# Optimization experiments

Hardware: AMD Instinct MI355X
Metric: run time of the kernel (lower is better)

## Reference

```python
import jax, jax.numpy as jnp
import numpy as np
from jax import lax

LEAKY_ALPHA = 0.2  # tf.nn.leaky_relu default


def setup_inputs() -> dict:
    key = jax.random.key(0)
    k1, k2, k3 = jax.random.split(key, 3)
    B, C, D, H, W = 8, 2, 96, 64, 64
    F, d, h, w = 8, 3, 60, 64
    inputs = jax.random.normal(k1, (B, C, D, H, W), dtype=jnp.float32)
    # weight/bias correspond to tf variables [F,1,c,d,h,w] with the singleton squeezed
    weight = jax.random.normal(k2, (F, C, d, h, w), dtype=jnp.float32) * 0.05
    bias = jax.random.normal(k3, (F, C, d, h, w), dtype=jnp.float32) * 0.05
    return {"inputs": inputs, "weight": weight, "bias": bias}


def reference(inputs, weight, bias):
    B, C, D, H, W = inputs.shape
    F, _, d, h, w = weight.shape
    margin = H - h
    Dout = D - d + 1  # depth positions where tf.slice succeeds

    # sliding depth windows: xwin[b,c,i,k,:,:] = inputs[b,c,i+k,:,:] -> [B,C,Dout,d,H,W]
    xwin = jnp.stack([inputs[:, :, k:k + Dout] for k in range(d)], axis=3)
    # margin accumulation over H (sum of margin+1 shifted h-slices): [B,C,Dout,d,h,W]
    s = xwin[..., 0:h, :]
    for j in range(1, margin + 1):
        s = s + xwin[..., j:j + h, :]
    s = jnp.moveaxis(s, 2, 1)  # [B,Dout,C,d,h,w]

    # y = (sum_j x_slice_j * w + b) * 0.25 -> a[b,f,i,c,k,p,q]
    a = (s[:, None] * weight[None, :, None] + bias[None, :, None]) * 0.25
    # a: [B,F,Dout,C,d,h,w]

    # fixed ones-kernel conv3d, filters=1, SAME, strides (d,1,1), then leaky_relu
    a_r = a.reshape(B * F * Dout, C, d, h, w)
    kernel = jnp.ones((1, C, 3, 3, 3), dtype=a_r.dtype)
    conv = lax.conv_general_dilated(
        a_r, kernel, window_strides=(d, 1, 1), padding='SAME',
        dimension_numbers=('NCDHW', 'OIDHW', 'NCDHW'))  # [N,1,1,h,w]
    out = jax.nn.leaky_relu(conv, negative_slope=LEAKY_ALPHA)
    return out.reshape(B, F, Dout, h, w)
```

## Files before the change

### kernel.cpp

```cpp
#include <hip/hip_runtime.h>

#define B_ 8
#define C_ 2
#define D_ 96
#define H_ 64
#define W_ 64
#define F_ 8
#define KD 3
#define h_ 60
#define Dout_ 94
#define PLANE (h_ * W_)
#define NCH (PLANE / 4)
#define TD 8
#define NTILE ((Dout_ + TD - 1) / TD)
#define S2_FLOATS ((size_t)B_ * C_ * D_ * PLANE)

__global__ __launch_bounds__(256) void k_s2(const float* __restrict__ in,
                                            float* __restrict__ s2) {
    const int bx = blockIdx.x;
    const float4* ip4 = (const float4*)(in + (size_t)bx * (H_ * W_));
    float4* op4 = (float4*)(s2 + (size_t)bx * PLANE);
    __shared__ float4 lds[H_ * 16];
    const int tid = threadIdx.x;
#pragma unroll
    for (int k = 0; k < 4; ++k) lds[tid + 256 * k] = ip4[tid + 256 * k];
    __syncthreads();
#pragma unroll
    for (int k = 0; k < 4; ++k) {
        const int e = tid + 256 * k;
        if (e < NCH) {
            const int row = e >> 4, col = e & 15;
            float4 s = lds[row * 16 + col];
#pragma unroll
            for (int j = 1; j < 5; ++j) {
                const float4 v = lds[(row + j) * 16 + col];
                s.x += v.x; s.y += v.y; s.z += v.z; s.w += v.w;
            }
            op4[e] = s;
        }
    }
}

__device__ __forceinline__ float4 hsum3(float4 V, int col4) {
    const int lane = threadIdx.x & 63;
    float lw = __shfl(V.w, (lane + 63) & 63, 64);
    float rx = __shfl(V.x, (lane + 1) & 63, 64);
    if (col4 == 0) lw = 0.f;
    if (col4 == 15) rx = 0.f;
    float4 o;
    o.x = lw + V.x + V.y;
    o.y = V.x + V.y + V.z;
    o.z = V.y + V.z + V.w;
    o.w = V.z + V.w + rx;
    return o;
}

__global__ __launch_bounds__(256) void k_boxbs(const float* __restrict__ bs,
                                               float* __restrict__ bb) {
    const int f = blockIdx.x;
    const int tid = threadIdx.x;
    __shared__ float4 R[62 * 16];
    if (tid < 32) {
        const int r = (tid >> 4) ? 61 : 0;
        R[r * 16 + (tid & 15)] = make_float4(0, 0, 0, 0);
    }
    const float4* bp = (const float4*)(bs + (size_t)f * (C_ * KD * PLANE));
#pragma unroll
    for (int k = 0; k < 4; ++k) {
        const int e = tid + 256 * k;
        if (e < NCH) {
            float4 s = make_float4(0, 0, 0, 0);
#pragma unroll
            for (int s6 = 0; s6 < 6; ++s6) {
                const float4 v = bp[s6 * NCH + e];
                s.x += v.x; s.y += v.y; s.z += v.z; s.w += v.w;
            }
            const int row = e >> 4, col = e & 15;
            R[(row + 1) * 16 + col] = s;
        }
    }
    __syncthreads();
    float4* ob = (float4*)(bb + (size_t)f * PLANE);
#pragma unroll
    for (int k = 0; k < 4; ++k) {
        const int e = tid + 256 * k;
        if (e < NCH) {
            const int row = e >> 4, c4 = e & 15;
            const float4 a = R[row * 16 + c4];
            const float4 m = R[(row + 1) * 16 + c4];
            const float4 d = R[(row + 2) * 16 + c4];
            float4 V;
            V.x = a.x + m.x + d.x; V.y = a.y + m.y + d.y;
            V.z = a.z + m.z + d.z; V.w = a.w + m.w + d.w;
            ob[e] = hsum3(V, c4);
        }
    }
}

__global__ __launch_bounds__(256) void k_main(const float* __restrict__ s2,
                                              const float* __restrict__ wt,
                                              const float* __restrict__ bb,
                                              float* __restrict__ out) {
    const int bx = blockIdx.x;
    const int tile = bx % NTILE;
    const int f = (bx / NTILE) % F_;
    const int b = bx / (NTILE * F_);
    const int d0 = tile * TD;
    const int tid = threadIdx.x;

    float4 wreg[6][4];
    const float4* wp = (const float4*)(wt + (size_t)f * (C_ * KD * PLANE));
#pragma unroll
    for (int s6 = 0; s6 < 6; ++s6)
#pragma unroll
        for (int k = 0; k < 4; ++k) {
            const int e = tid + 256 * k;
            wreg[s6][k] = (e < NCH) ? wp[s6 * NCH + e] : make_float4(0, 0, 0, 0);
        }

    __shared__ float4 R[62 * 16];
    if (tid < 32) {
        const int r = (tid >> 4) ? 61 : 0;
        R[r * 16 + (tid & 15)] = make_float4(0, 0, 0, 0);
    }

    const float4* s2b = (const float4*)s2 + (size_t)(b * C_) * D_ * NCH;
    const float4* bbp = (const float4*)(bb + (size_t)f * PLANE);
    float* ob = out + (size_t)((b * F_ + f) * Dout_) * PLANE;

    for (int t = 0; t < TD; ++t) {
        const int dout = d0 + t;
        if (dout >= Dout_) break;

        float4 acc[4];
#pragma unroll
        for (int k = 0; k < 4; ++k) acc[k] = make_float4(0, 0, 0, 0);

#pragma unroll
        for (int c = 0; c < C_; ++c)
#pragma unroll
            for (int z = 0; z < KD; ++z) {
                const float4* sp = s2b + (size_t)(c * D_ + dout + z) * NCH;
#pragma unroll
                for (int k = 0; k < 4; ++k) {
                    const int e = tid + 256 * k;
                    if (e < NCH) {
                        const float4 v = sp[e];
                        const float4 w = wreg[c * KD + z][k];
                        acc[k].x += v.x * w.x; acc[k].y += v.y * w.y;
                        acc[k].z += v.z * w.z; acc[k].w += v.w * w.w;
                    }
                }
            }

        if (t > 0) __syncthreads();
#pragma unroll
        for (int k = 0; k < 4; ++k) {
            const int e = tid + 256 * k;
            if (e < NCH) R[((e >> 4) + 1) * 16 + (e & 15)] = acc[k];
        }
        __syncthreads();

        float4* od4 = (float4*)(ob + (size_t)dout * PLANE);
#pragma unroll
        for (int k = 0; k < 4; ++k) {
            const int e = tid + 256 * k;
            if (e < NCH) {
                const int row = e >> 4, c4 = e & 15;
                const float4 a = R[row * 16 + c4];
                const float4 m = R[(row + 1) * 16 + c4];
                const float4 d = R[(row + 2) * 16 + c4];
                float4 V;
                V.x = a.x + m.x + d.x; V.y = a.y + m.y + d.y;
                V.z = a.z + m.z + d.z; V.w = a.w + m.w + d.w;
                float4 o = hsum3(V, c4);
                const float4 bbv = bbp[e];
                o.x = 0.25f * (o.x + bbv.x); o.y = 0.25f * (o.y + bbv.y);
                o.z = 0.25f * (o.z + bbv.z); o.w = 0.25f * (o.w + bbv.w);
                o.x = (o.x > 0.f) ? o.x : 0.2f * o.x;
                o.y = (o.y > 0.f) ? o.y : 0.2f * o.y;
                o.z = (o.z > 0.f) ? o.z : 0.2f * o.z;
                o.w = (o.w > 0.f) ? o.w : 0.2f * o.w;
                od4[e] = o;
            }
        }
    }
}

extern "C" void kernel_launch(void* const* d_in, const int* in_sizes, int n_in,
                              void* d_out, int out_size, void* d_ws, size_t ws_size,
                              hipStream_t stream) {
    const float* in = (const float*)d_in[0];
    const float* wt = (const float*)d_in[1];
    const float* bs = (const float*)d_in[2];
    float* out = (float*)d_out;

    float* s2 = (float*)d_ws;
    float* bb = s2 + S2_FLOATS;

    k_boxbs<<<dim3(F_), dim3(256), 0, stream>>>(bs, bb);
    k_s2<<<dim3(B_ * C_ * D_), dim3(256), 0, stream>>>(in, s2);
    k_main<<<dim3(B_ * F_ * NTILE), dim3(256), 0, stream>>>(s2, wt, bb, out);
}
```

Measured before the change: 168.4 us.

## Merge prep kernels, halve depth tile, double-buffer LDS and unroll main loop

Merges the s2 box-sum kernel and the bias box-filter kernel into one launch that dispatches on block index, which removes one kernel launch. In the main kernel, the depth tile drops from 8 to 4, giving twice as many blocks for more parallelism but more per-block weight register loads. The LDS staging buffer is double-buffered, so one barrier per step replaces two. The depth loop is fully unrolled with clamped reads instead of an early break. The cost is redundant weight reloads per block and extra clamped compute on the tail tile.

Result: no change. 165.2 us (-1.9%).

```diff
diff --git a/kernel.cpp b/kernel.cpp
--- a/kernel.cpp
+++ b/kernel.cpp
@@ -11,35 +11,10 @@
 #define Dout_ 94
 #define PLANE (h_ * W_)
 #define NCH (PLANE / 4)
-#define TD 8
+#define TD 4
 #define NTILE ((Dout_ + TD - 1) / TD)
-#define S2_FLOATS ((size_t)B_ * C_ * D_ * PLANE)
-
-__global__ __launch_bounds__(256) void k_s2(const float* __restrict__ in,
-                                            float* __restrict__ s2) {
-    const int bx = blockIdx.x;
-    const float4* ip4 = (const float4*)(in + (size_t)bx * (H_ * W_));
-    float4* op4 = (float4*)(s2 + (size_t)bx * PLANE);
-    __shared__ float4 lds[H_ * 16];
-    const int tid = threadIdx.x;
-#pragma unroll
-    for (int k = 0; k < 4; ++k) lds[tid + 256 * k] = ip4[tid + 256 * k];
-    __syncthreads();
-#pragma unroll
-    for (int k = 0; k < 4; ++k) {
-        const int e = tid + 256 * k;
-        if (e < NCH) {
-            const int row = e >> 4, col = e & 15;
-            float4 s = lds[row * 16 + col];
-#pragma unroll
-            for (int j = 1; j < 5; ++j) {
-                const float4 v = lds[(row + j) * 16 + col];
-                s.x += v.x; s.y += v.y; s.z += v.z; s.w += v.w;
-            }
-            op4[e] = s;
-        }
-    }
-}
+#define NS2 (B_ * C_ * D_)
+#define S2_FLOATS ((size_t)NS2 * PLANE)
 
 __device__ __forceinline__ float4 hsum3(float4 V, int col4) {
     const int lane = threadIdx.x & 63;
@@ -55,44 +30,70 @@
     return o;
 }
 
-__global__ __launch_bounds__(256) void k_boxbs(const float* __restrict__ bs,
-                                               float* __restrict__ bb) {
-    const int f = blockIdx.x;
+__global__ __launch_bounds__(256) void k_prep(const float* __restrict__ in,
+                                              const float* __restrict__ bs,
+                                              float* __restrict__ s2,
+                                              float* __restrict__ bb) {
+    const int bx = blockIdx.x;
     const int tid = threadIdx.x;
-    __shared__ float4 R[62 * 16];
-    if (tid < 32) {
-        const int r = (tid >> 4) ? 61 : 0;
-        R[r * 16 + (tid & 15)] = make_float4(0, 0, 0, 0);
-    }
-    const float4* bp = (const float4*)(bs + (size_t)f * (C_ * KD * PLANE));
-#pragma unroll
-    for (int k = 0; k < 4; ++k) {
-        const int e = tid + 256 * k;
-        if (e < NCH) {
-            float4 s = make_float4(0, 0, 0, 0);
-#pragma unroll
-            for (int s6 = 0; s6 < 6; ++s6) {
-                const float4 v = bp[s6 * NCH + e];
-                s.x += v.x; s.y += v.y; s.z += v.z; s.w += v.w;
-            }
-            const int row = e >> 4, col = e & 15;
-            R[(row + 1) * 16 + col] = s;
-        }
-    }
-    __syncthreads();
-    float4* ob = (float4*)(bb + (size_t)f * PLANE);
-#pragma unroll
-    for (int k = 0; k < 4; ++k) {
-        const int e = tid + 256 * k;
-        if (e < NCH) {
-            const int row = e >> 4, c4 = e & 15;
-            const float4 a = R[row * 16 + c4];
-            const float4 m = R[(row + 1) * 16 + c4];
-            const float4 d = R[(row + 2) * 16 + c4];
-            float4 V;
-            V.x = a.x + m.x + d.x; V.y = a.y + m.y + d.y;
-            V.z = a.z + m.z + d.z; V.w = a.w + m.w + d.w;
-            ob[e] = hsum3(V, c4);
+    __shared__ float4 lds[H_ * 16];
+
+    if (bx < NS2) {
+        const float4* ip4 = (const float4*)(in + (size_t)bx * (H_ * W_));
+        float4* op4 = (float4*)(s2 + (size_t)bx * PLANE);
+#pragma unroll
+        for (int k = 0; k < 4; ++k) lds[tid + 256 * k] = ip4[tid + 256 * k];
+        __syncthreads();
+#pragma unroll
+        for (int k = 0; k < 4; ++k) {
+            const int e = tid + 256 * k;
+            if (e < NCH) {
+                const int row = e >> 4, col = e & 15;
+                float4 s = lds[row * 16 + col];
+#pragma unroll
+                for (int j = 1; j < 5; ++j) {
+                    const float4 v = lds[(row + j) * 16 + col];
+                    s.x += v.x; s.y += v.y; s.z += v.z; s.w += v.w;
+                }
+                op4[e] = s;
+            }
+        }
+    } else {
+        const int f = bx - NS2;
+        float4* R = lds;
+        if (tid < 32) {
+            const int r = (tid >> 4) ? 61 : 0;
+            R[r * 16 + (tid & 15)] = make_float4(0, 0, 0, 0);
+        }
+        const float4* bp = (const float4*)(bs + (size_t)f * (C_ * KD * PLANE));
+#pragma unroll
+        for (int k = 0; k < 4; ++k) {
+            const int e = tid + 256 * k;
+            if (e < NCH) {
+                float4 s = make_float4(0, 0, 0, 0);
+#pragma unroll
+                for (int s6 = 0; s6 < 6; ++s6) {
+                    const float4 v = bp[s6 * NCH + e];
+                    s.x += v.x; s.y += v.y; s.z += v.z; s.w += v.w;
+                }
+                R[((e >> 4) + 1) * 16 + (e & 15)] = s;
+            }
+        }
+        __syncthreads();
+        float4* ob = (float4*)(bb + (size_t)f * PLANE);
+#pragma unroll
+        for (int k = 0; k < 4; ++k) {
+            const int e = tid + 256 * k;
+            if (e < NCH) {
+                const int row = e >> 4, c4 = e & 15;
+                const float4 a = R[row * 16 + c4];
+                const float4 m = R[(row + 1) * 16 + c4];
+                const float4 d = R[(row + 2) * 16 + c4];
+                float4 V;
+                V.x = a.x + m.x + d.x; V.y = a.y + m.y + d.y;
+                V.z = a.z + m.z + d.z; V.w = a.w + m.w + d.w;
+                ob[e] = hsum3(V, c4);
+            }
         }
     }
 }
@@ -118,19 +119,20 @@
             wreg[s6][k] = (e < NCH) ? wp[s6 * NCH + e] : make_float4(0, 0, 0, 0);
         }
 
-    __shared__ float4 R[62 * 16];
+    __shared__ float4 R[2][62 * 16];
     if (tid < 32) {
         const int r = (tid >> 4) ? 61 : 0;
-        R[r * 16 + (tid & 15)] = make_float4(0, 0, 0, 0);
+        R[0][r * 16 + (tid & 15)] = make_float4(0, 0, 0, 0);
+        R[1][r * 16 + (tid & 15)] = make_float4(0, 0, 0, 0);
     }
 
     const float4* s2b = (const float4*)s2 + (size_t)(b * C_) * D_ * NCH;
     const float4* bbp = (const float4*)(bb + (size_t)f * PLANE);
     float* ob = out + (size_t)((b * F_ + f) * Dout_) * PLANE;
 
+#pragma unroll
     for (int t = 0; t < TD; ++t) {
         const int dout = d0 + t;
-        if (dout >= Dout_) break;
 
         float4 acc[4];
 #pragma unroll
@@ -140,7 +142,8 @@
         for (int c = 0; c < C_; ++c)
 #pragma unroll
             for (int z = 0; z < KD; ++z) {
-                const float4* sp = s2b + (size_t)(c * D_ + dout + z) * NCH;
+                int p = dout + z; if (p > D_ - 1) p = D_ - 1;
+                const float4* sp = s2b + (size_t)(c * D_ + p) * NCH;
 #pragma unroll
                 for (int k = 0; k < 4; ++k) {
                     const int e = tid + 256 * k;
@@ -153,35 +156,37 @@
                 }
             }
 
-        if (t > 0) __syncthreads();
-#pragma unroll
-        for (int k = 0; k < 4; ++k) {
-            const int e = tid + 256 * k;
-            if (e < NCH) R[((e >> 4) + 1) * 16 + (e & 15)] = acc[k];
+        float4* Rb = R[t & 1];
+#pragma unroll
+        for (int k = 0; k < 4; ++k) {
+            const int e = tid + 256 * k;
+            if (e < NCH) Rb[((e >> 4) + 1) * 16 + (e & 15)] = acc[k];
         }
         __syncthreads();
 
-        float4* od4 = (float4*)(ob + (size_t)dout * PLANE);
-#pragma unroll
-        for (int k = 0; k < 4; ++k) {
-            const int e = tid + 256 * k;
-            if (e < NCH) {
-                const int row = e >> 4, c4 = e & 15;
-                const float4 a = R[row * 16 + c4];
-                const float4 m = R[(row + 1) * 16 + c4];
-                const float4 d = R[(row + 2) * 16 + c4];
-                float4 V;
-                V.x = a.x + m.x + d.x; V.y = a.y + m.y + d.y;
-                V.z = a.z + m.z + d.z; V.w = a.w + m.w + d.w;
-                float4 o = hsum3(V, c4);
-                const float4 bbv = bbp[e];
-                o.x = 0.25f * (o.x + bbv.x); o.y = 0.25f * (o.y + bbv.y);
-                o.z = 0.25f * (o.z + bbv.z); o.w = 0.25f * (o.w + bbv.w);
-                o.x = (o.x > 0.f) ? o.x : 0.2f * o.x;
-                o.y = (o.y > 0.f) ? o.y : 0.2f * o.y;
-                o.z = (o.z > 0.f) ? o.z : 0.2f * o.z;
-                o.w = (o.w > 0.f) ? o.w : 0.2f * o.w;
-                od4[e] = o;
+        if (dout < Dout_) {
+            float4* od4 = (float4*)(ob + (size_t)dout * PLANE);
+#pragma unroll
+            for (int k = 0; k < 4; ++k) {
+                const int e = tid + 256 * k;
+                if (e < NCH) {
+                    const int row = e >> 4, c4 = e & 15;
+                    const float4 a = Rb[row * 16 + c4];
+                    const float4 m = Rb[(row + 1) * 16 + c4];
+                    const float4 d = Rb[(row + 2) * 16 + c4];
+                    float4 V;
+                    V.x = a.x + m.x + d.x; V.y = a.y + m.y + d.y;
+                    V.z = a.z + m.z + d.z; V.w = a.w + m.w + d.w;
+                    float4 o = hsum3(V, c4);
+                    const float4 bbv = bbp[e];
+                    o.x = 0.25f * (o.x + bbv.x); o.y = 0.25f * (o.y + bbv.y);
+                    o.z = 0.25f * (o.z + bbv.z); o.w = 0.25f * (o.w + bbv.w);
+                    o.x = (o.x > 0.f) ? o.x : 0.2f * o.x;
+                    o.y = (o.y > 0.f) ? o.y : 0.2f * o.y;
+                    o.z = (o.z > 0.f) ? o.z : 0.2f * o.z;
+                    o.w = (o.w > 0.f) ? o.w : 0.2f * o.w;
+                    od4[e] = o;
+                }
             }
         }
     }
@@ -198,7 +203,6 @@
     float* s2 = (float*)d_ws;
     float* bb = s2 + S2_FLOATS;
 
-    k_boxbs<<<dim3(F_), dim3(256), 0, stream>>>(bs, bb);
-    k_s2<<<dim3(B_ * C_ * D_), dim3(256), 0, stream>>>(in, s2);
+    k_prep<<<dim3(NS2 + F_), dim3(256), 0, stream>>>(in, bs, s2, bb);
     k_main<<<dim3(B_ * F_ * NTILE), dim3(256), 0, stream>>>(s2, wt, bb, out);
 }
```

## Fuse margin-sum into main kernel and parallelize over batch and depth position

Applied to the files above, without the earlier changes.

The separate kernel that wrote the H-margin sums to a workspace is removed. The main kernel now loads each input plane into LDS, forms the margin sums in registers, and uses one 320-thread block per (batch, output depth). Each block loops over all filters and reads weights from global memory, ping-ponging two LDS buffers between the plane loads and the 3x3 box stage. This drops the workspace write and re-read and one launch. In exchange the full weight tensor is streamed through cache by every block, and the shuffle in the bias-box kernel now runs unconditionally so all lanes take part.

New measurement: 253.3 us. 50.4% more time.

```diff
diff --git a/kernel.cpp b/kernel.cpp
--- a/kernel.cpp
+++ b/kernel.cpp
@@ -11,42 +11,26 @@
 #define Dout_ 94
 #define PLANE (h_ * W_)
 #define NCH (PLANE / 4)
-#define TD 8
-#define NTILE ((Dout_ + TD - 1) / TD)
-#define S2_FLOATS ((size_t)B_ * C_ * D_ * PLANE)
+#define INCH (H_ * W_ / 4)
+#define NT 320
 
-__global__ __launch_bounds__(256) void k_s2(const float* __restrict__ in,
-                                            float* __restrict__ s2) {
-    const int bx = blockIdx.x;
-    const float4* ip4 = (const float4*)(in + (size_t)bx * (H_ * W_));
-    float4* op4 = (float4*)(s2 + (size_t)bx * PLANE);
-    __shared__ float4 lds[H_ * 16];
-    const int tid = threadIdx.x;
-#pragma unroll
-    for (int k = 0; k < 4; ++k) lds[tid + 256 * k] = ip4[tid + 256 * k];
-    __syncthreads();
-#pragma unroll
-    for (int k = 0; k < 4; ++k) {
-        const int e = tid + 256 * k;
-        if (e < NCH) {
-            const int row = e >> 4, col = e & 15;
-            float4 s = lds[row * 16 + col];
-#pragma unroll
-            for (int j = 1; j < 5; ++j) {
-                const float4 v = lds[(row + j) * 16 + col];
-                s.x += v.x; s.y += v.y; s.z += v.z; s.w += v.w;
-            }
-            op4[e] = s;
-        }
-    }
+__device__ __forceinline__ float4 f4fma(float4 a, float4 b, float4 c) {
+    c.x += a.x * b.x; c.y += a.y * b.y; c.z += a.z * b.z; c.w += a.w * b.w;
+    return c;
+}
+__device__ __forceinline__ float4 f4add3(float4 a, float4 b, float4 c) {
+    float4 o;
+    o.x = a.x + b.x + c.x; o.y = a.y + b.y + c.y;
+    o.z = a.z + b.z + c.z; o.w = a.w + b.w + c.w;
+    return o;
 }
 
-__device__ __forceinline__ float4 hsum3(float4 V, int col4) {
+__device__ __forceinline__ float4 hsum3(float4 V, int c4) {
     const int lane = threadIdx.x & 63;
     float lw = __shfl(V.w, (lane + 63) & 63, 64);
     float rx = __shfl(V.x, (lane + 1) & 63, 64);
-    if (col4 == 0) lw = 0.f;
-    if (col4 == 15) rx = 0.f;
+    if (c4 == 0) lw = 0.f;
+    if (c4 == 15) rx = 0.f;
     float4 o;
     o.x = lw + V.x + V.y;
     o.y = V.x + V.y + V.z;
@@ -55,8 +39,8 @@
     return o;
 }
 
-__global__ __launch_bounds__(256) void k_boxbs(const float* __restrict__ bs,
-                                               float* __restrict__ bb) {
+__global__ __launch_bounds__(256) void k_bb(const float* __restrict__ bs,
+                                            float* __restrict__ bb) {
     const int f = blockIdx.x;
     const int tid = threadIdx.x;
     __shared__ float4 R[62 * 16];
@@ -75,8 +59,7 @@
                 const float4 v = bp[s6 * NCH + e];
                 s.x += v.x; s.y += v.y; s.z += v.z; s.w += v.w;
             }
-            const int row = e >> 4, col = e & 15;
-            R[(row + 1) * 16 + col] = s;
+            R[((e >> 4) + 1) * 16 + (e & 15)] = s;
         }
     }
     __syncthreads();
@@ -84,105 +67,117 @@
 #pragma unroll
     for (int k = 0; k < 4; ++k) {
         const int e = tid + 256 * k;
+        float4 V = make_float4(0, 0, 0, 0);
+        int c4 = e & 15;
         if (e < NCH) {
-            const int row = e >> 4, c4 = e & 15;
-            const float4 a = R[row * 16 + c4];
-            const float4 m = R[(row + 1) * 16 + c4];
-            const float4 d = R[(row + 2) * 16 + c4];
-            float4 V;
-            V.x = a.x + m.x + d.x; V.y = a.y + m.y + d.y;
-            V.z = a.z + m.z + d.z; V.w = a.w + m.w + d.w;
-            ob[e] = hsum3(V, c4);
+            const int row = e >> 4;
+            V = f4add3(R[row * 16 + c4], R[(row + 1) * 16 + c4],
+                       R[(row + 2) * 16 + c4]);
         }
+        float4 o = hsum3(V, c4);
+        if (e < NCH) ob[e] = o;
     }
 }
 
-__global__ __launch_bounds__(256) void k_main(const float* __restrict__ s2,
-                                              const float* __restrict__ wt,
-                                              const float* __restrict__ bb,
-                                              float* __restrict__ out) {
+__global__ __launch_bounds__(NT) void k_main(const float* __restrict__ in,
+                                             const float* __restrict__ wt,
+                                             const float* __restrict__ bb,
+                                             float* __restrict__ out) {
     const int bx = blockIdx.x;
-    const int tile = bx % NTILE;
-    const int f = (bx / NTILE) % F_;
-    const int b = bx / (NTILE * F_);
-    const int d0 = tile * TD;
+    const int dout = bx % Dout_;
+    const int b = bx / Dout_;
     const int tid = threadIdx.x;
 
-    float4 wreg[6][4];
-    const float4* wp = (const float4*)(wt + (size_t)f * (C_ * KD * PLANE));
+    __shared__ float4 L[2][INCH];
+
+    int e[3], c4[3], row[3];
 #pragma unroll
-    for (int s6 = 0; s6 < 6; ++s6)
+    for (int k = 0; k < 3; ++k) {
+        e[k] = tid + NT * k;
+        row[k] = e[k] >> 4;
+        c4[k] = e[k] & 15;
+    }
+
+    float4 s2r[6][3];
+    const float4* in4 = (const float4*)in;
 #pragma unroll
-        for (int k = 0; k < 4; ++k) {
-            const int e = tid + 256 * k;
-            wreg[s6][k] = (e < NCH) ? wp[s6 * NCH + e] : make_float4(0, 0, 0, 0);
+    for (int c = 0; c < C_; ++c)
+#pragma unroll
+        for (int z = 0; z < KD; ++z) {
+            const int p = c * KD + z;
+            const size_t pb = ((size_t)(b * C_ + c) * D_ + (dout + z)) * INCH;
+            float4* Ls = L[p & 1];
+#pragma unroll
+            for (int k2 = 0; k2 < 4; ++k2) {
+                const int idx = tid + NT * k2;
+                if (idx < INCH) Ls[idx] = in4[pb + idx];
+            }
+            __syncthreads();
+#pragma unroll
+            for (int k = 0; k < 3; ++k) {
+                float4 s = Ls[row[k] * 16 + c4[k]];
+#pragma unroll
+                for (int j = 1; j < 5; ++j) {
+                    const float4 v = Ls[(row[k] + j) * 16 + c4[k]];
+                    s.x += v.x; s.y += v.y; s.z += v.z; s.w += v.w;
+                }
+                s2r[p][k] = s;
+            }
         }
 
-    __shared__ float4 R[62 * 16];
-    if (tid < 32) {
-        const int r = (tid >> 4) ? 61 : 0;
-        R[r * 16 + (tid & 15)] = make_float4(0, 0, 0, 0);
-    }
+    const float4* wt4 = (const float4*)wt;
+    const float4* bb4 = (const float4*)bb;
+    float4* out4 = (float4*)out;
+    const float4 z4 = make_float4(0, 0, 0, 0);
 
-    const float4* s2b = (const float4*)s2 + (size_t)(b * C_) * D_ * NCH;
-    const float4* bbp = (const float4*)(bb + (size_t)f * PLANE);
-    float* ob = out + (size_t)((b * F_ + f) * Dout_) * PLANE;
-
-    for (int t = 0; t < TD; ++t) {
-        const int dout = d0 + t;
-        if (dout >= Dout_) break;
-
-        float4 acc[4];
+    for (int f = 0; f < F_; ++f) {
+        float4 acc[3];
 #pragma unroll
-        for (int k = 0; k < 4; ++k) acc[k] = make_float4(0, 0, 0, 0);
+        for (int k = 0; k < 3; ++k) acc[k] = z4;
 
 #pragma unroll
         for (int c = 0; c < C_; ++c)
 #pragma unroll
             for (int z = 0; z < KD; ++z) {
-                const float4* sp = s2b + (size_t)(c * D_ + dout + z) * NCH;
+                const size_t wb = (size_t)((f * C_ + c) * KD + z) * NCH;
 #pragma unroll
-                for (int k = 0; k < 4; ++k) {
-                    const int e = tid + 256 * k;
-                    if (e < NCH) {
-                        const float4 v = sp[e];
-                        const float4 w = wreg[c * KD + z][k];
-                        acc[k].x += v.x * w.x; acc[k].y += v.y * w.y;
-                        acc[k].z += v.z * w.z; acc[k].w += v.w * w.w;
-                    }
+                for (int k = 0; k < 3; ++k) {
+                    const float4 w = wt4[wb + e[k]];
+                    acc[k] = f4fma(w, s2r[c * KD + z][k], acc[k]);
                 }
             }
 
-        if (t > 0) __syncthreads();
+        float4 bbv[3];
 #pragma unroll
-        for (int k = 0; k < 4; ++k) {
-            const int e = tid + 256 * k;
-            if (e < NCH) R[((e >> 4) + 1) * 16 + (e & 15)] = acc[k];
+        for (int k = 0; k < 3; ++k)
+            bbv[k] = bb4[(size_t)f * NCH + e[k]];
+
+        float4* Lb = L[f & 1];
+        if (f < 2 && tid < 32) {
+            const int r = (tid >> 4) ? 61 : 0;
+            Lb[r * 16 + (tid & 15)] = z4;
         }
+#pragma unroll
+        for (int k = 0; k < 3; ++k)
+            Lb[(row[k] + 1) * 16 + c4[k]] = acc[k];
         __syncthreads();
 
-        float4* od4 = (float4*)(ob + (size_t)dout * PLANE);
+        const size_t ob = ((size_t)(b * F_ + f) * Dout_ + dout) * NCH;
 #pragma unroll
-        for (int k = 0; k < 4; ++k) {
-            const int e = tid + 256 * k;
-            if (e < NCH) {
-                const int row = e >> 4, c4 = e & 15;
-                const float4 a = R[row * 16 + c4];
-                const float4 m = R[(row + 1) * 16 + c4];
-                const float4 d = R[(row + 2) * 16 + c4];
-                float4 V;
-                V.x = a.x + m.x + d.x; V.y = a.y + m.y + d.y;
-                V.z = a.z + m.z + d.z; V.w = a.w + m.w + d.w;
-                float4 o = hsum3(V, c4);
-                const float4 bbv = bbp[e];
-                o.x = 0.25f * (o.x + bbv.x); o.y = 0.25f * (o.y + bbv.y);
-                o.z = 0.25f * (o.z + bbv.z); o.w = 0.25f * (o.w + bbv.w);
-                o.x = (o.x > 0.f) ? o.x : 0.2f * o.x;
-                o.y = (o.y > 0.f) ? o.y : 0.2f * o.y;
-                o.z = (o.z > 0.f) ? o.z : 0.2f * o.z;
-                o.w = (o.w > 0.f) ? o.w : 0.2f * o.w;
-                od4[e] = o;
-            }
+        for (int k = 0; k < 3; ++k) {
+            const float4 V = f4add3(Lb[row[k] * 16 + c4[k]],
+                                    Lb[(row[k] + 1) * 16 + c4[k]],
+                                    Lb[(row[k] + 2) * 16 + c4[k]]);
+            float4 o = hsum3(V, c4[k]);
+            o.x = 0.25f * (o.x + bbv[k].x);
+            o.y = 0.25f * (o.y + bbv[k].y);
+            o.z = 0.25f * (o.z + bbv[k].z);
+            o.w = 0.25f * (o.w + bbv[k].w);
+            o.x = (o.x > 0.f) ? o.x : 0.2f * o.x;
+            o.y = (o.y > 0.f) ? o.y : 0.2f * o.y;
+            o.z = (o.z > 0.f) ? o.z : 0.2f * o.z;
+            o.w = (o.w > 0.f) ? o.w : 0.2f * o.w;
+            out4[ob + e[k]] = o;
         }
     }
 }
@@ -194,11 +189,8 @@
     const float* wt = (const float*)d_in[1];
     const float* bs = (const float*)d_in[2];
     float* out = (float*)d_out;
+    float* bb = (float*)d_ws;
 
-    float* s2 = (float*)d_ws;
-    float* bb = s2 + S2_FLOATS;
-
-    k_boxbs<<<dim3(F_), dim3(256), 0, stream>>>(bs, bb);
-    k_s2<<<dim3(B_ * C_ * D_), dim3(256), 0, stream>>>(in, s2);
-    k_main<<<dim3(B_ * F_ * NTILE), dim3(256), 0, stream>>>(s2, wt, bb, out);
+    k_bb<<<dim3(F_), dim3(256), 0, stream>>>(bs, bb);
+    k_main<<<dim3(B_ * Dout_), dim3(NT), 0, stream>>>(in, wt, bb, out);
 }
```
